# Optimization experiments

Hardware: AMD Instinct MI355X
Metric: run time of the kernel (lower is better)

## Reference

```python
import math
import jax, jax.numpy as jnp
import numpy as np

B, T, D, K, R, KC = 4, 2048, 1024, 8, 16, 4
H = 4 * D  # mlp hidden


def setup_inputs() -> dict:
    key = jax.random.key(0)
    ks = jax.random.split(key, 12)
    s = lambda i, shape: jax.random.normal(ks[i], shape, jnp.float32) * 0.02
    # state_decay_logit init: geometric decays in [dmin, dmax], logit = log(p) - log1p(-p)
    dmin, dmax = 0.9, 0.999
    dec = np.exp(np.linspace(math.log(dmin), math.log(dmax), K))
    decay_logit = jnp.asarray(np.log(dec) - np.log1p(-dec), jnp.float32)
    return dict(
        x=jax.random.normal(ks[0], (B, T, D), jnp.float32),
        conv_w=s(1, (D, 1, KC)),            # depthwise conv kernel (torch Conv1d weight)
        gp_w=s(2, (D, D)), gp_b=jnp.zeros((D,), jnp.float32),
        up_w=s(3, (D, H)), up_b=jnp.zeros((H,), jnp.float32),
        dn_w=s(4, (H, D)), dn_b=jnp.zeros((D,), jnp.float32),
        si_w=s(5, (D, K * D)),              # state_in (no bias)
        so_w=s(6, (K * D, D)),              # state_out (no bias)
        decay_logit=decay_logit,
        rs_w=s(7, (D, R)), rs_b=jnp.zeros((R,), jnp.float32),
        rwg_w=s(8, (D, 1)), rwg_b=jnp.zeros((1,), jnp.float32),
        rv_w=s(9, (D, D)), rv_b=jnp.zeros((D,), jnp.float32),
        gr_w=s(10, (D, 1)), gr_b=jnp.zeros((1,), jnp.float32),
        gl_w=s(11, (D, 1)), gl_b=jnp.zeros((1,), jnp.float32),
    )


def _rms_norm(x, eps=1e-6):
    return x * jax.lax.rsqrt(jnp.mean(x * x, axis=-1, keepdims=True) + eps)


def _forward(x, conv_w, gp_w, gp_b, up_w, up_b, dn_w, dn_b, si_w, so_w,
             decay_logit, rs_w, rs_b, rwg_w, rwg_b, rv_w, rv_b, gr_w, gr_b, gl_w, gl_b):
    Bx, Tx, Dx = x.shape
    u = _rms_norm(x)
    # --- local mixer: causal depthwise conv + sigmoid gate + SiLU MLP ---
    xc = jax.lax.conv_general_dilated(
        jnp.swapaxes(u, 1, 2), conv_w, window_strides=(1,),
        padding=[(KC - 1, 0)], feature_group_count=Dx,
        dimension_numbers=('NCH', 'OIH', 'NCH'))
    xc = jnp.swapaxes(xc, 1, 2)                       # (B,T,D) causal conv output
    xg = xc * jax.nn.sigmoid(xc @ gp_w + gp_b)
    local = jax.nn.silu(xg @ up_w + up_b) @ dn_w + dn_b
    # --- per-channel exponential-decay state + register read/write scan ---
    dec = jax.nn.sigmoid(decay_logit)                 # (K,)
    z = (u @ si_w).reshape(Bx, Tx, K, Dx)             # state_in, (B,T,K,D)
    sel = jax.nn.softmax(u @ rs_w + rs_b, axis=-1)    # soft register address (B,T,R)
    wg = jax.nn.sigmoid(u @ rwg_w + rwg_b)            # write gate (B,T,1)
    v = u @ rv_w + rv_b                                # register value (B,T,D)

    def step(carry, inp):
        s, regs = carry
        z_t, sel_t, w_t, v_t = inp
        read = jnp.einsum('br,brd->bd', sel_t, regs)  # soft read before write
        ws = (w_t * sel_t)[:, :, None]                # (B,R,1)
        regs = regs * (1.0 - ws) + ws * v_t[:, None, :]
        s = dec[None, :, None] * s + z_t
        return (s, regs), (s, read)

    init = (jnp.zeros((Bx, K, Dx), x.dtype), jnp.zeros((Bx, R, Dx), x.dtype))
    tm = lambda a: jnp.swapaxes(a, 0, 1)              # time-major for scan
    _, (s_all, reads) = jax.lax.scan(step, init, (tm(z), tm(sel), tm(wg), tm(v)))
    s_all = tm(s_all)                                 # (B,T,K,D)
    reads = tm(reads)                                 # (B,T,D)
    long_out = jnp.einsum('btkd,kde->bte', s_all, so_w.reshape(K, Dx, Dx))
    g_long = jax.nn.sigmoid(u @ gl_w + gl_b)
    g_reg = jax.nn.sigmoid(u @ gr_w + gr_b)
    return x + local + g_long * long_out + g_reg * reads


def reference(x, conv_w, gp_w, gp_b, up_w, up_b, dn_w, dn_b, si_w, so_w,
              decay_logit, rs_w, rs_b, rwg_w, rwg_b, rv_w, rv_b, gr_w, gr_b, gl_w, gl_b):
    return _forward(x, conv_w, gp_w, gp_b, up_w, up_b, dn_w, dn_b, si_w, so_w,
                    decay_logit, rs_w, rs_b, rwg_w, rwg_b, rv_w, rv_b, gr_w, gr_b, gl_w, gl_b)
```

## Files before the change

### kernel.cpp

```cpp
#include <hip/hip_runtime.h>

typedef unsigned short u16;
typedef __bf16 bf16x8 __attribute__((ext_vector_type(8)));
typedef float f32x4 __attribute__((ext_vector_type(4)));
typedef u16 u16x4 __attribute__((ext_vector_type(4)));

#define D_ 1024
#define T_ 2048
#define B_ 4
#define K_ 8
#define R_ 16
#define H_ 4096
#define NROW (B_*T_)
#define CH 32
#define CL (T_/CH)
#define CHS 64
#define CLS (T_/CHS)

__device__ __forceinline__ u16 f2bf(float f){
  union{float f;unsigned u;} v; v.f=f;
  unsigned r = v.u + 0x7FFFu + ((v.u>>16)&1u);
  return (u16)(r>>16);
}
__device__ __forceinline__ float bf2f(u16 b){
  union{unsigned u;float f;} v; v.u = ((unsigned)b)<<16; return v.f;
}
__device__ __forceinline__ float sigm(float x){ return 1.f/(1.f+__expf(-x)); }

__device__ __forceinline__ void gload_lds16(const void* g, void* l){
  __builtin_amdgcn_global_load_lds((const __attribute__((address_space(1))) void*)g,
                                   (__attribute__((address_space(3))) void*)l, 16, 0, 0);
}

__global__ __launch_bounds__(256) void fill_k(float* __restrict__ out, long n, float v){
  long i = (long)blockIdx.x*256 + threadIdx.x;
  if (i < n) out[i] = v;
}

__global__ __launch_bounds__(256) void transpose_cast(const float* __restrict__ in, u16* __restrict__ out,
                                                      int R, int C){
  __shared__ float tile[32][33];
  int bx = blockIdx.x*32;
  int by = blockIdx.y*32;
  int tx = threadIdx.x & 31, ty = threadIdx.x >> 5;
  #pragma unroll
  for (int i=0;i<32;i+=8) tile[ty+i][tx] = in[(size_t)(by+ty+i)*C + bx+tx];
  __syncthreads();
  #pragma unroll
  for (int i=0;i<32;i+=8) out[(size_t)(bx+ty+i)*R + by+tx] = f2bf(tile[tx][ty+i]);
}

__global__ __launch_bounds__(256) void castbf(const float* __restrict__ in, u16* __restrict__ out, long n){
  long i = (long)blockIdx.x*256 + threadIdx.x;
  if (i < n) out[i] = f2bf(in[i]);
}

__global__ __launch_bounds__(256) void initout_k(const float* __restrict__ x, const float* __restrict__ b,
                                                 float* __restrict__ out){
  size_t i = ((size_t)blockIdx.x*256 + threadIdx.x)*4;
  f32x4 xv = *(const f32x4*)(x + i);
  f32x4 bv = *(const f32x4*)(b + (i & (D_-1)));
  xv += bv;
  *(f32x4*)(out + i) = xv;
}

__global__ __launch_bounds__(256) void rmsnorm_k(const float* __restrict__ x, u16* __restrict__ u){
  int row = blockIdx.x;
  const float* xr = x + (size_t)row*D_;
  float xv[4]; float ss = 0.f;
  #pragma unroll
  for (int i=0;i<4;i++){ xv[i] = xr[threadIdx.x + 256*i]; ss += xv[i]*xv[i]; }
  #pragma unroll
  for (int o=32;o>0;o>>=1) ss += __shfl_down(ss, o);
  __shared__ float red[4];
  if ((threadIdx.x&63)==0) red[threadIdx.x>>6] = ss;
  __syncthreads();
  float tot = red[0]+red[1]+red[2]+red[3];
  float r = rsqrtf(tot*(1.f/D_) + 1e-6f);
  #pragma unroll
  for (int i=0;i<4;i++) u[(size_t)row*D_ + threadIdx.x + 256*i] = f2bf(xv[i]*r);
}

__global__ __launch_bounds__(256) void conv_k(const u16* __restrict__ u, const float* __restrict__ w,
                                              u16* __restrict__ xc){
  size_t base = ((size_t)blockIdx.x*256 + threadIdx.x)*4;
  int t  = (int)((base >> 10) & (T_-1));
  int d0 = (int)(base & (D_-1));
  f32x4 wv[4];
  #pragma unroll
  for (int jj=0;jj<4;jj++) wv[jj] = *(const f32x4*)&w[(d0+jj)*4];
  float acc[4] = {0.f,0.f,0.f,0.f};
  #pragma unroll
  for (int j=0;j<4;j++){
    if (t-3+j >= 0){
      u16x4 uv = *(const u16x4*)(u + base + (long)(j-3)*D_);
      #pragma unroll
      for (int jj=0;jj<4;jj++) acc[jj] += bf2f(uv[jj]) * wv[jj][j];
    }
  }
  u16x4 o;
  #pragma unroll
  for (int jj=0;jj<4;jj++) o[jj] = f2bf(acc[jj]);
  *(u16x4*)(xc + base) = o;
}

__global__ __launch_bounds__(256) void smalln_k(const u16* __restrict__ u,
    const float* __restrict__ rs_w, const float* __restrict__ rs_b,
    const float* __restrict__ rwg_w, const float* __restrict__ rwg_b,
    const float* __restrict__ gl_w, const float* __restrict__ gl_b,
    const float* __restrict__ gr_w, const float* __restrict__ gr_b,
    float* __restrict__ sel, float* __restrict__ wg, float* __restrict__ gl, float* __restrict__ gr){
  int row = blockIdx.x, tid = threadIdx.x;
  float p[19];
  #pragma unroll
  for (int c=0;c<19;c++) p[c] = 0.f;
  for (int i=0;i<4;i++){
    int e = tid + i*256;
    float ue = bf2f(u[(size_t)row*D_ + e]);
    const float* rw = rs_w + (size_t)e*16;
    #pragma unroll
    for (int r=0;r<16;r++) p[r] += ue*rw[r];
    p[16] += ue*rwg_w[e];
    p[17] += ue*gl_w[e];
    p[18] += ue*gr_w[e];
  }
  __shared__ float red[19*4];
  #pragma unroll
  for (int c=0;c<19;c++){
    float v = p[c];
    #pragma unroll
    for (int o=32;o>0;o>>=1) v += __shfl_down(v, o);
    if ((tid&63)==0) red[c*4 + (tid>>6)] = v;
  }
  __syncthreads();
  if (tid==0){
    float s[19];
    #pragma unroll
    for (int c=0;c<19;c++) s[c] = red[c*4]+red[c*4+1]+red[c*4+2]+red[c*4+3];
    float mx = -1e30f;
    #pragma unroll
    for (int r=0;r<16;r++){ s[r] += rs_b[r]; mx = fmaxf(mx, s[r]); }
    float ssum = 0.f;
    #pragma unroll
    for (int r=0;r<16;r++){ s[r] = __expf(s[r]-mx); ssum += s[r]; }
    float inv = 1.f/ssum;
    #pragma unroll
    for (int r=0;r<16;r++) sel[(size_t)row*16+r] = s[r]*inv;
    wg[row] = sigm(s[16] + rwg_b[0]);
    gl[row] = sigm(s[17] + gl_b[0]);
    gr[row] = sigm(s[18] + gr_b[0]);
  }
}

#define BM 128
#define BN 128
#define BK 32

template<int EPI>
__global__ __launch_bounds__(256)
void gemm_bt(const u16* __restrict__ A, const u16* __restrict__ BT,
             void* __restrict__ outp, const float* __restrict__ bias,
             const void* __restrict__ aux,
             int K, int lda, int ldb, int ldc,
             long zA, long zB, long zC)
{
  __shared__ __attribute__((aligned(16))) u16 As[BM*BK];
  __shared__ __attribute__((aligned(16))) u16 Bs[BN*BK];
  int nwg = gridDim.x*gridDim.y;
  int bx = blockIdx.x, by = blockIdx.y;
  if ((nwg & 7) == 0){
    int bid = blockIdx.y*gridDim.x + blockIdx.x;
    int cpx = nwg >> 3;
    int s = (bid & 7)*cpx + (bid >> 3);
    bx = s % gridDim.x; by = s / gridDim.x;
  }
  const u16* Ab = A + (size_t)blockIdx.z*zA + (size_t)bx*BM*lda;
  const u16* Bb = BT + (size_t)blockIdx.z*zB + (size_t)by*BN*ldb;
  int tid = threadIdx.x, lane = tid&63, wid = tid>>6;
  int wr = wid>>1, wc = wid&1;
  f32x4 acc[4][4];
  #pragma unroll
  for (int m=0;m<4;m++)
    #pragma unroll
    for (int n=0;n<4;n++) acc[m][n] = (f32x4){0.f,0.f,0.f,0.f};

  int srow = lane>>2;
  int scol = (lane&3)*8;
  int klo  = (lane>>4)*8;
  for (int k0=0; k0<K; k0+=BK){
    #pragma unroll
    for (int i=0;i<2;i++){
      int r0 = wid*32 + i*16;
      gload_lds16(Ab + (size_t)(r0+srow)*lda + k0 + scol, &As[r0*BK]);
      gload_lds16(Bb + (size_t)(r0+srow)*ldb + k0 + scol, &Bs[r0*BK]);
    }
    __syncthreads();
    bf16x8 af[4], bfr[4];
    #pragma unroll
    for (int m=0;m<4;m++) af[m] = *(const bf16x8*)&As[(wr*64+m*16+(lane&15))*BK + klo];
    #pragma unroll
    for (int n=0;n<4;n++) bfr[n] = *(const bf16x8*)&Bs[(wc*64+n*16+(lane&15))*BK + klo];
    #pragma unroll
    for (int m=0;m<4;m++)
      #pragma unroll
      for (int n=0;n<4;n++)
        acc[m][n] = __builtin_amdgcn_mfma_f32_16x16x32_bf16(af[m], bfr[n], acc[m][n], 0, 0, 0);
    __syncthreads();
  }

  size_t obase = (size_t)blockIdx.z*zC;
  int row0 = bx*BM + wr*64;
  int col0 = by*BN + wc*64;
  #pragma unroll
  for (int m=0;m<4;m++){
    #pragma unroll
    for (int n=0;n<4;n++){
      int col = col0 + n*16 + (lane&15);
      #pragma unroll
      for (int r=0;r<4;r++){
        int row = row0 + m*16 + (lane>>4)*4 + r;
        float c = acc[m][n][r];
        size_t idx = obase + (size_t)row*ldc + col;
        if (EPI==0){ ((u16*)outp)[idx] = f2bf(c); }
        else if (EPI==1){ ((u16*)outp)[idx] = f2bf(c + bias[col]); }
        else if (EPI==2){ float t=c+bias[col]; ((u16*)outp)[idx] = f2bf(bf2f(((const u16*)aux)[idx]) * sigm(t)); }
        else if (EPI==3){ float t=c+bias[col]; ((u16*)outp)[idx] = f2bf(t*sigm(t)); }
        else if (EPI==4){ ((float*)outp)[idx] = ((const float*)aux)[idx] + c + bias[col]; }
        else            { ((float*)outp)[idx] += c; }
      }
    }
  }
}

template<int NT, int EPI>
__global__ __launch_bounds__(512, 2)
void gemm8p(const u16* __restrict__ A, const u16* __restrict__ BT,
            void* __restrict__ outp, const float* __restrict__ bias,
            const void* __restrict__ aux,
            int lda, int ldb, int ldc, long zA, long zB, long zC,
            int rx, int ry, int nry)
{
  __shared__ __attribute__((aligned(16))) u16 lds8[65536];
  int bid = blockIdx.y*gridDim.x + blockIdx.x;
  int xcd = bid & 7;
  int s   = bid >> 3;
  int rgx = xcd / nry, rgy = xcd - rgx*nry;
  int bx = rgx*rx + (s % rx);
  int by = rgy*ry + (s / rx);

  const u16* Ab = A + (size_t)blockIdx.z*zA + (size_t)bx*256*lda;
  const u16* Bb = BT + (size_t)blockIdx.z*zB + (size_t)by*256*ldb;

  int tid = threadIdx.x, l = tid&63, w = tid>>6;
  int wr = w>>2, wc = w&3;
  int rS0 = (w*2+0)*8 + (l>>3);
  int rS1 = (w*2+1)*8 + (l>>3);
  int cg  = (((l&7) ^ (l>>3)) << 3);
  int seg0 = (w*2+0)*512;
  int seg1 = (w*2+1)*512;

  auto STAGE = [&](int h){
    int kt = h>>2, idx = h&3, par = kt&1;
    int koff = kt*64;
    if (idx < 2){
      const u16* s0 = Bb + (size_t)(idx*128 + rS0)*ldb + koff + cg;
      const u16* s1 = Bb + (size_t)(idx*128 + rS1)*ldb + koff + cg;
      u16* d = &lds8[par*32768 + 16384 + idx*8192];
      gload_lds16(s0, d + seg0);
      gload_lds16(s1, d + seg1);
    } else {
      int a = idx-2;
      const u16* s0 = Ab + (size_t)(a*128 + rS0)*lda + koff + cg;
      const u16* s1 = Ab + (size_t)(a*128 + rS1)*lda + koff + cg;
      u16* d = &lds8[par*32768 + a*8192];
      gload_lds16(s0, d + seg0);
      gload_lds16(s1, d + seg1);
    }
  };

  f32x4 acc[8][4];
  #pragma unroll
  for (int m=0;m<8;m++)
    #pragma unroll
    for (int n=0;n<4;n++) acc[m][n] = (f32x4){0.f,0.f,0.f,0.f};

  for (int h=0; h<7; ++h) STAGE(h);
  asm volatile("s_waitcnt vmcnt(6)" ::: "memory");
  __builtin_amdgcn_s_barrier();

  for (int it=0; it<NT/2; ++it){
    #pragma unroll
    for (int sub=0; sub<2; ++sub){
      int kt = it*2+sub;
      const int par = sub;
      u16* Abase = &lds8[par*32768 + wr*8192];
      u16* Bbase = &lds8[par*32768 + 16384 + (wc>>1)*8192];
      bf16x8 bf[4][2];
      #pragma unroll
      for (int q=0; q<4; ++q){
        bf16x8 af[2][2];
        if (q==0){
          #pragma unroll
          for (int n=0;n<4;n++)
            #pragma unroll
            for (int ss=0;ss<2;ss++){
              int rr = (wc&1)*64 + n*16 + (l&15);
              int c16 = (l>>4) + ss*4;
              bf[n][ss] = *(const bf16x8*)&Bbase[rr*64 + ((c16 ^ (rr&7))<<3)];
            }
        }
        #pragma unroll
        for (int i=0;i<2;i++)
          #pragma unroll
          for (int ss=0;ss<2;ss++){
            int rr = q*32 + i*16 + (l&15);
            int c16 = (l>>4) + ss*4;
            af[i][ss] = *(const bf16x8*)&Abase[rr*64 + ((c16 ^ (rr&7))<<3)];
          }
        __builtin_amdgcn_sched_barrier(0);
        int h = kt*4 + q + 7;
        if (h < 4*NT) STAGE(h);
        __builtin_amdgcn_s_barrier();
        asm volatile("s_waitcnt lgkmcnt(0)" ::: "memory");
        __builtin_amdgcn_sched_barrier(0);
        __builtin_amdgcn_s_setprio(1);
        #pragma unroll
        for (int i=0;i<2;i++)
          #pragma unroll
          for (int n=0;n<4;n++)
            #pragma unroll
            for (int ss=0;ss<2;ss++)
              acc[q*2+i][n] = __builtin_amdgcn_mfma_f32_16x16x32_bf16(af[i][ss], bf[n][ss], acc[q*2+i][n], 0, 0, 0);
        __builtin_amdgcn_s_setprio(0);
        if (q==3){
          if (kt == NT-2)      asm volatile("s_waitcnt vmcnt(0)" ::: "memory");
          else if (kt < NT-2)  asm volatile("s_waitcnt vmcnt(6)" ::: "memory");
        }
        __builtin_amdgcn_s_barrier();
      }
    }
  }

  size_t obase = (size_t)blockIdx.z*zC;
  int row0 = bx*256 + wr*128;
  int col0 = by*256 + wc*64;
  #pragma unroll
  for (int m=0;m<8;m++){
    #pragma unroll
    for (int n=0;n<4;n++){
      int col = col0 + n*16 + (l&15);
      #pragma unroll
      for (int r=0;r<4;r++){
        int row = row0 + m*16 + (l>>4)*4 + r;
        float c = acc[m][n][r];
        size_t idx = obase + (size_t)row*ldc + col;
        if (EPI==0){ ((u16*)outp)[idx] = f2bf(c); }
        else if (EPI==1){ ((u16*)outp)[idx] = f2bf(c + bias[col]); }
        else if (EPI==2){ float t=c+bias[col]; ((u16*)outp)[idx] = f2bf(bf2f(((const u16*)aux)[idx]) * sigm(t)); }
        else if (EPI==3){ float t=c+bias[col]; ((u16*)outp)[idx] = f2bf(t*sigm(t)); }
        else            { unsafeAtomicAdd(&((float*)outp)[idx], c); }
      }
    }
  }
}

template<int NT>
__global__ __launch_bounds__(512, 2)
void gemm8z(const u16* __restrict__ A, const u16* __restrict__ BT,
            void* __restrict__ outp, const float* __restrict__ bias,
            const float* __restrict__ bias2, const void* __restrict__ aux,
            int lda, int ldb, int ldc, long zA, long zB, long zC,
            int rx, int ry, int nry)
{
  __shared__ __attribute__((aligned(16))) u16 lds8[65536];
  int bid = blockIdx.y*gridDim.x + blockIdx.x;
  int xcd = bid & 7;
  int s   = bid >> 3;
  int rgx = xcd / nry, rgy = xcd - rgx*nry;
  int bx = rgx*rx + (s % rx);
  int by = rgy*ry + (s / rx);

  const u16* Ab = A + (size_t)blockIdx.z*zA + (size_t)bx*256*lda;
  const u16* Bb = BT + (size_t)blockIdx.z*zB + (size_t)by*256*ldb;

  int tid = threadIdx.x, l = tid&63, w = tid>>6;
  int wr = w>>2, wc = w&3;
  int rS0 = (w*2+0)*8 + (l>>3);
  int rS1 = (w*2+1)*8 + (l>>3);
  int cg  = (((l&7) ^ (l>>3)) << 3);
  int seg0 = (w*2+0)*512;
  int seg1 = (w*2+1)*512;

  auto STAGE = [&](int h){
    int kt = h>>2, idx = h&3, par = kt&1;
    int koff = kt*64;
    if (idx < 2){
      const u16* s0 = Bb + (size_t)(idx*128 + rS0)*ldb + koff + cg;
      const u16* s1 = Bb + (size_t)(idx*128 + rS1)*ldb + koff + cg;
      u16* d = &lds8[par*32768 + 16384 + idx*8192];
      gload_lds16(s0, d + seg0);
      gload_lds16(s1, d + seg1);
    } else {
      int a = idx-2;
      const u16* s0 = Ab + (size_t)(a*128 + rS0)*lda + koff + cg;
      const u16* s1 = Ab + (size_t)(a*128 + rS1)*lda + koff + cg;
      u16* d = &lds8[par*32768 + a*8192];
      gload_lds16(s0, d + seg0);
      gload_lds16(s1, d + seg1);
    }
  };

  f32x4 acc[8][4];
  #pragma unroll
  for (int m=0;m<8;m++)
    #pragma unroll
    for (int n=0;n<4;n++) acc[m][n] = (f32x4){0.f,0.f,0.f,0.f};

  for (int h=0; h<7; ++h) STAGE(h);
  asm volatile("s_waitcnt vmcnt(6)" ::: "memory");
  __builtin_amdgcn_s_barrier();

  for (int it=0; it<NT/2; ++it){
    #pragma unroll
    for (int sub=0; sub<2; ++sub){
      int kt = it*2+sub;
      const int par = sub;
      u16* Abase = &lds8[par*32768 + wr*8192];
      u16* Bbase = &lds8[par*32768 + 16384 + (wc>>1)*8192];
      bf16x8 bf[4][2];
      #pragma unroll
      for (int q=0; q<4; ++q){
        bf16x8 af[2][2];
        if (q==0){
          #pragma unroll
          for (int n=0;n<4;n++)
            #pragma unroll
            for (int ss=0;ss<2;ss++){
              int rr = (wc&1)*64 + n*16 + (l&15);
              int c16 = (l>>4) + ss*4;
              bf[n][ss] = *(const bf16x8*)&Bbase[rr*64 + ((c16 ^ (rr&7))<<3)];
            }
        }
        #pragma unroll
        for (int i=0;i<2;i++)
          #pragma unroll
          for (int ss=0;ss<2;ss++){
            int rr = q*32 + i*16 + (l&15);
            int c16 = (l>>4) + ss*4;
            af[i][ss] = *(const bf16x8*)&Abase[rr*64 + ((c16 ^ (rr&7))<<3)];
          }
        __builtin_amdgcn_sched_barrier(0);
        int h = kt*4 + q + 7;
        if (h < 4*NT) STAGE(h);
        __builtin_amdgcn_s_barrier();
        asm volatile("s_waitcnt lgkmcnt(0)" ::: "memory");
        __builtin_amdgcn_sched_barrier(0);
        __builtin_amdgcn_s_setprio(1);
        #pragma unroll
        for (int i=0;i<2;i++)
          #pragma unroll
          for (int n=0;n<4;n++)
            #pragma unroll
            for (int ss=0;ss<2;ss++)
              acc[q*2+i][n] = __builtin_amdgcn_mfma_f32_16x16x32_bf16(af[i][ss], bf[n][ss], acc[q*2+i][n], 0, 0, 0);
        __builtin_amdgcn_s_setprio(0);
        if (q==3){
          if (kt == NT-2)      asm volatile("s_waitcnt vmcnt(0)" ::: "memory");
          else if (kt < NT-2)  asm volatile("s_waitcnt vmcnt(6)" ::: "memory");
        }
        __builtin_amdgcn_s_barrier();
      }
    }
  }

  size_t obase = (size_t)blockIdx.z*zC;
  int row0 = bx*256 + wr*128;
  int col0 = by*256 + wc*64;
  bool z0 = (blockIdx.z == 0);
  #pragma unroll
  for (int m=0;m<8;m++){
    #pragma unroll
    for (int n=0;n<4;n++){
      int col = col0 + n*16 + (l&15);
      #pragma unroll
      for (int r=0;r<4;r++){
        int row = row0 + m*16 + (l>>4)*4 + r;
        float c = acc[m][n][r];
        size_t idx = obase + (size_t)row*ldc + col;
        if (z0){ float t=c+bias[col]; ((u16*)outp)[idx] = f2bf(bf2f(((const u16*)aux)[idx]) * sigm(t)); }
        else   { ((u16*)outp)[idx] = f2bf(c + bias2[col]); }
      }
    }
  }
}

template<int NT, int EPI>
__global__ __launch_bounds__(512, 2)
void gemm4p(const u16* __restrict__ A, const u16* __restrict__ BT,
            void* __restrict__ outp, const float* __restrict__ bias,
            const void* __restrict__ aux,
            int lda, int ldb, int ldc, long zA, long zB, long zC,
            int rx, int ry, int nry)
{
  __shared__ __attribute__((aligned(16))) u16 lds8[65536];
  int bid = blockIdx.y*gridDim.x + blockIdx.x;
  int xcd = bid & 7;
  int s   = bid >> 3;
  int rgx = xcd / nry, rgy = xcd - rgx*nry;
  int bx = rgx*rx + (s % rx);
  int by = rgy*ry + (s / rx);

  const u16* Ab = A + (size_t)blockIdx.z*zA + (size_t)bx*256*lda;
  const u16* Bb = BT + (size_t)blockIdx.z*zB + (size_t)by*256*ldb;

  int tid = threadIdx.x, l = tid&63, w = tid>>6;
  int wr = w>>2, wc = w&3;
  int rS0 = (w*2+0)*8 + (l>>3);
  int rS1 = (w*2+1)*8 + (l>>3);
  int cg  = (((l&7) ^ (l>>3)) << 3);
  int seg0 = (w*2+0)*512;
  int seg1 = (w*2+1)*512;

  auto STAGE = [&](int h){
    if (h >= 4*NT) return;
    int kt = h>>2, idx = h&3, par = kt&1;
    int koff = kt*64;
    if (idx < 2){
      const u16* s0 = Bb + (size_t)(idx*128 + rS0)*ldb + koff + cg;
      const u16* s1 = Bb + (size_t)(idx*128 + rS1)*ldb + koff + cg;
      u16* d = &lds8[par*32768 + 16384 + idx*8192];
      gload_lds16(s0, d + seg0);
      gload_lds16(s1, d + seg1);
    } else {
      int a = idx-2;
      const u16* s0 = Ab + (size_t)(a*128 + rS0)*lda + koff + cg;
      const u16* s1 = Ab + (size_t)(a*128 + rS1)*lda + koff + cg;
      u16* d = &lds8[par*32768 + a*8192];
      gload_lds16(s0, d + seg0);
      gload_lds16(s1, d + seg1);
    }
  };

  f32x4 acc[8][4];
  #pragma unroll
  for (int m=0;m<8;m++)
    #pragma unroll
    for (int n=0;n<4;n++) acc[m][n] = (f32x4){0.f,0.f,0.f,0.f};

  for (int h=0; h<7; ++h) STAGE(h);
  asm volatile("s_waitcnt vmcnt(6)" ::: "memory");
  __builtin_amdgcn_s_barrier();

  for (int kt=0; kt<NT; ++kt){
    const int par = kt&1;
    u16* Abase = &lds8[par*32768 + wr*8192];
    u16* Bbase = &lds8[par*32768 + 16384 + (wc>>1)*8192];
    bf16x8 bf[4][2];
    #pragma unroll
    for (int n=0;n<4;n++)
      #pragma unroll
      for (int ss=0;ss<2;ss++){
        int rr = (wc&1)*64 + n*16 + (l&15);
        int c16 = (l>>4) + ss*4;
        bf[n][ss] = *(const bf16x8*)&Bbase[rr*64 + ((c16 ^ (rr&7))<<3)];
      }
    bf16x8 afA[2][2][2];
    #pragma unroll
    for (int qq=0;qq<2;qq++)
      #pragma unroll
      for (int i=0;i<2;i++)
        #pragma unroll
        for (int ss=0;ss<2;ss++){
          int rr = qq*32 + i*16 + (l&15);
          int c16 = (l>>4) + ss*4;
          afA[qq][i][ss] = *(const bf16x8*)&Abase[rr*64 + ((c16 ^ (rr&7))<<3)];
        }
    STAGE(kt*4 + 7);
    STAGE(kt*4 + 8);
    __builtin_amdgcn_s_barrier();
    asm volatile("s_waitcnt lgkmcnt(0)" ::: "memory");
    __builtin_amdgcn_sched_barrier(0);
    __builtin_amdgcn_s_setprio(1);
    #pragma unroll
    for (int qq=0;qq<2;qq++)
      #pragma unroll
      for (int i=0;i<2;i++)
        #pragma unroll
        for (int n=0;n<4;n++)
          #pragma unroll
          for (int ss=0;ss<2;ss++)
            acc[qq*2+i][n] = __builtin_amdgcn_mfma_f32_16x16x32_bf16(afA[qq][i][ss], bf[n][ss], acc[qq*2+i][n], 0, 0, 0);
    __builtin_amdgcn_s_setprio(0);
    __builtin_amdgcn_s_barrier();
    bf16x8 afB[2][2][2];
    #pragma unroll
    for (int qq=0;qq<2;qq++)
      #pragma unroll
      for (int i=0;i<2;i++)
        #pragma unroll
        for (int ss=0;ss<2;ss++){
          int rr = (qq+2)*32 + i*16 + (l&15);
          int c16 = (l>>4) + ss*4;
          afB[qq][i][ss] = *(const bf16x8*)&Abase[rr*64 + ((c16 ^ (rr&7))<<3)];
        }
    STAGE(kt*4 + 9);
    STAGE(kt*4 + 10);
    __builtin_amdgcn_s_barrier();
    asm volatile("s_waitcnt lgkmcnt(0)" ::: "memory");
    __builtin_amdgcn_sched_barrier(0);
    __builtin_amdgcn_s_setprio(1);
    #pragma unroll
    for (int qq=0;qq<2;qq++)
      #pragma unroll
      for (int i=0;i<2;i++)
        #pragma unroll
        for (int n=0;n<4;n++)
          #pragma unroll
          for (int ss=0;ss<2;ss++)
            acc[(qq+2)*2+i][n] = __builtin_amdgcn_mfma_f32_16x16x32_bf16(afB[qq][i][ss], bf[n][ss], acc[(qq+2)*2+i][n], 0, 0, 0);
    __builtin_amdgcn_s_setprio(0);
    if (kt == NT-2)      asm volatile("s_waitcnt vmcnt(0)" ::: "memory");
    else if (kt < NT-2)  asm volatile("s_waitcnt vmcnt(6)" ::: "memory");
    __builtin_amdgcn_s_barrier();
  }

  size_t obase = (size_t)blockIdx.z*zC;
  int row0 = bx*256 + wr*128;
  int col0 = by*256 + wc*64;
  #pragma unroll
  for (int m=0;m<8;m++){
    #pragma unroll
    for (int n=0;n<4;n++){
      int col = col0 + n*16 + (l&15);
      #pragma unroll
      for (int r=0;r<4;r++){
        int row = row0 + m*16 + (l>>4)*4 + r;
        float c = acc[m][n][r];
        size_t idx = obase + (size_t)row*ldc + col;
        if (EPI==0){ ((u16*)outp)[idx] = f2bf(c); }
        else if (EPI==1){ ((u16*)outp)[idx] = f2bf(c + bias[col]); }
        else if (EPI==3){ float t=c+bias[col]; ((u16*)outp)[idx] = f2bf(t*sigm(t)); }
        else            { unsafeAtomicAdd(&((float*)outp)[idx], c); }
      }
    }
  }
}

template<int KH>
__global__ __launch_bounds__(256) void scan_s1k(const u16* __restrict__ y, const float* __restrict__ logit,
                                                int p, float* __restrict__ Hend){
  int k = blockIdx.x;
  int e0 = threadIdx.x*4;
  int c = blockIdx.y, b = blockIdx.z;
  float dec = sigm(logit[KH*p+k]);
  f32x4 h = (f32x4){0.f,0.f,0.f,0.f};
  size_t row0 = (size_t)b*T_ + (size_t)c*CLS;
  for (int t=0;t<CLS;t++){
    u16x4 w = *(const u16x4*)(y + (row0+t)*(size_t)(KH*D_) + (size_t)k*D_ + e0);
    #pragma unroll
    for (int j=0;j<4;j++) h[j] = dec*h[j] + bf2f(w[j]);
  }
  *(f32x4*)&Hend[(((size_t)b*CHS+c)*KH+k)*D_ + e0] = h;
}

template<int KH>
__global__ __launch_bounds__(256) void scan_s2v(const float* __restrict__ Hend, const float* __restrict__ logit,
                                                int p, float* __restrict__ Sinit){
  int idx = blockIdx.x*256 + threadIdx.x;
  if (idx >= B_*KH*D_) return;
  int e = idx % D_; int kh = (idx/D_) % KH; int b = idx/(D_*KH);
  float dec = sigm(logit[KH*p+kh]);
  float dL = powf(dec, (float)CLS);
  float carry = 0.f;
  for (int c=0;c<CHS;c++){
    size_t i3 = (((size_t)b*CHS+c)*KH+kh)*D_ + e;
    Sinit[i3] = carry;
    carry = dL*carry + Hend[i3];
  }
}

template<int KH>
__global__ __launch_bounds__(128) void scan_s3v(const u16* __restrict__ y, const float* __restrict__ logit,
                                                int p, const float* __restrict__ Sinit,
                                                const float* __restrict__ glb, float* __restrict__ out){
  int e0 = (blockIdx.x*128 + threadIdx.x)*4;
  int c = blockIdx.y, b = blockIdx.z;
  float dec[KH]; f32x4 h[KH];
  #pragma unroll
  for (int k=0;k<KH;k++){
    dec[k] = sigm(logit[KH*p+k]);
    h[k] = *(const f32x4*)&Sinit[(((size_t)b*CHS+c)*KH+k)*D_ + e0];
  }
  size_t row0 = (size_t)b*T_ + (size_t)c*CLS;
  for (int t=0;t<CLS;t++){
    const u16* yp = y + (row0+t)*(size_t)(KH*D_) + e0;
    f32x4 sum = (f32x4){0.f,0.f,0.f,0.f};
    #pragma unroll
    for (int k=0;k<KH;k++){
      u16x4 w = *(const u16x4*)(yp + (size_t)k*D_);
      #pragma unroll
      for (int j=0;j<4;j++){ h[k][j] = dec[k]*h[k][j] + bf2f(w[j]); sum[j] += h[k][j]; }
    }
    float g = glb[row0+t];
    f32x4* op = (f32x4*)&out[(row0+t)*D_ + e0];
    f32x4 ov = *op;
    #pragma unroll
    for (int j=0;j<4;j++) ov[j] += g*sum[j];
    *op = ov;
  }
}

__global__ __launch_bounds__(256) void scan_r1(const u16* __restrict__ v, const float* __restrict__ sel,
                                               const float* __restrict__ wg,
                                               float* __restrict__ Rend, float* __restrict__ Pout){
  int d = blockIdx.x*256 + threadIdx.x;
  int c = blockIdx.y, b = blockIdx.z;
  __shared__ float sel_s[CL*R_];
  __shared__ float wg_s[CL];
  size_t row0 = (size_t)b*T_ + (size_t)c*CL;
  for (int i=threadIdx.x; i<CL*R_; i+=256) sel_s[i] = sel[row0*R_ + i];
  for (int i=threadIdx.x; i<CL;    i+=256) wg_s[i]  = wg[row0 + i];
  __syncthreads();
  float regs[R_], P[R_];
  #pragma unroll
  for (int r=0;r<R_;r++){ regs[r]=0.f; P[r]=1.f; }
  for (int t=0;t<CL;t++){
    float vv = bf2f(v[(row0+t)*D_ + d]);
    float w = wg_s[t];
    #pragma unroll
    for (int r=0;r<R_;r++){
      float ws = w*sel_s[t*R_+r];
      regs[r] += ws*(vv - regs[r]);
      P[r] *= (1.f - ws);
    }
  }
  #pragma unroll
  for (int r=0;r<R_;r++) Rend[(((size_t)b*CH+c)*R_+r)*D_ + d] = regs[r];
  if (blockIdx.x==0 && threadIdx.x==0){
    #pragma unroll
    for (int r=0;r<R_;r++) Pout[((size_t)b*CH+c)*R_ + r] = P[r];
  }
}

__global__ __launch_bounds__(256) void scan_r2(const float* __restrict__ Rend, const float* __restrict__ Pbuf,
                                               float* __restrict__ Rinit){
  int idx = blockIdx.x*256 + threadIdx.x;
  if (idx >= B_*D_) return;
  int d = idx % D_; int b = idx / D_;
  float regs[R_];
  #pragma unroll
  for (int r=0;r<R_;r++) regs[r] = 0.f;
  for (int c=0;c<CH;c++){
    #pragma unroll
    for (int r=0;r<R_;r++){
      size_t i3 = (((size_t)b*CH+c)*R_+r)*D_ + d;
      Rinit[i3] = regs[r];
      regs[r] = Pbuf[((size_t)b*CH+c)*R_+r]*regs[r] + Rend[i3];
    }
  }
}

__global__ __launch_bounds__(256) void scan_r3(const u16* __restrict__ v, const float* __restrict__ sel,
                                               const float* __restrict__ wg, const float* __restrict__ Rinit,
                                               const float* __restrict__ grb, float* __restrict__ out){
  int d = blockIdx.x*256 + threadIdx.x;
  int c = blockIdx.y, b = blockIdx.z;
  __shared__ float sel_s[CL*R_];
  __shared__ float wg_s[CL];
  size_t row0 = (size_t)b*T_ + (size_t)c*CL;
  for (int i=threadIdx.x; i<CL*R_; i+=256) sel_s[i] = sel[row0*R_ + i];
  for (int i=threadIdx.x; i<CL;    i+=256) wg_s[i]  = wg[row0 + i];
  __syncthreads();
  float regs[R_];
  #pragma unroll
  for (int r=0;r<R_;r++) regs[r] = Rinit[(((size_t)b*CH+c)*R_+r)*D_ + d];
  for (int t=0;t<CL;t++){
    float vv = bf2f(v[(row0+t)*D_ + d]);
    float w = wg_s[t];
    float read = 0.f;
    #pragma unroll
    for (int r=0;r<R_;r++){
      float sr = sel_s[t*R_+r];
      read += sr*regs[r];
      float ws = w*sr;
      regs[r] += ws*(vv - regs[r]);
    }
    out[(row0+t)*D_ + d] += grb[row0+t]*read;
  }
}

static void launch_gemm(int epi, dim3 g, const u16* A, const u16* BT, void* out,
                        const float* bias, const void* aux, int K, int lda, int ldb, int ldc,
                        long zA, long zB, long zC, hipStream_t s){
  switch(epi){
    case 0: gemm_bt<0><<<g,256,0,s>>>(A,BT,out,bias,aux,K,lda,ldb,ldc,zA,zB,zC); break;
    case 1: gemm_bt<1><<<g,256,0,s>>>(A,BT,out,bias,aux,K,lda,ldb,ldc,zA,zB,zC); break;
    case 2: gemm_bt<2><<<g,256,0,s>>>(A,BT,out,bias,aux,K,lda,ldb,ldc,zA,zB,zC); break;
    case 3: gemm_bt<3><<<g,256,0,s>>>(A,BT,out,bias,aux,K,lda,ldb,ldc,zA,zB,zC); break;
    case 4: gemm_bt<4><<<g,256,0,s>>>(A,BT,out,bias,aux,K,lda,ldb,ldc,zA,zB,zC); break;
    default: gemm_bt<5><<<g,256,0,s>>>(A,BT,out,bias,aux,K,lda,ldb,ldc,zA,zB,zC); break;
  }
}

extern "C" void kernel_launch(void* const* d_in, const int* in_sizes, int n_in,
                              void* d_out, int out_size, void* d_ws, size_t ws_size,
                              hipStream_t stream){
  const float* x      = (const float*)d_in[0];
  const float* conv_w = (const float*)d_in[1];
  const float* gp_w   = (const float*)d_in[2];
  const float* gp_b   = (const float*)d_in[3];
  const float* up_w   = (const float*)d_in[4];
  const float* up_b   = (const float*)d_in[5];
  const float* dn_w   = (const float*)d_in[6];
  const float* dn_b   = (const float*)d_in[7];
  const float* si_w   = (const float*)d_in[8];
  const float* so_w   = (const float*)d_in[9];
  const float* logit  = (const float*)d_in[10];
  const float* rs_w   = (const float*)d_in[11];
  const float* rs_b   = (const float*)d_in[12];
  const float* rwg_w  = (const float*)d_in[13];
  const float* rwg_b  = (const float*)d_in[14];
  const float* rv_w   = (const float*)d_in[15];
  const float* rv_b   = (const float*)d_in[16];
  const float* gr_w   = (const float*)d_in[17];
  const float* gr_b   = (const float*)d_in[18];
  const float* gl_w   = (const float*)d_in[19];
  const float* gl_b   = (const float*)d_in[20];
  float* out = (float*)d_out;
  char* base = (char*)d_ws;

  {
    size_t off = 0;
    auto al = [&](size_t b)->char*{ char* r = base+off; off += (b+255)&~(size_t)255; return r; };
    char* u_r    = al((size_t)NROW*D_*2);
    char* v_r    = al((size_t)NROW*D_*2);
    char* big    = al((size_t)121634816);
    float* sel   = (float*)al((size_t)NROW*R_*4);
    float* wgb   = (float*)al((size_t)NROW*4);
    float* glb   = (float*)al((size_t)NROW*4);
    float* grb   = (float*)al((size_t)NROW*4);
    float* Pbuf  = (float*)al((size_t)B_*CH*R_*4);
    float* Rend  = (float*)al((size_t)B_*CH*R_*D_*4);
    float* Rinit = (float*)al((size_t)B_*CH*R_*D_*4);
    if (off <= ws_size){
      u16* u_bf  = (u16*)u_r;
      u16* v_bf  = (u16*)v_r;
      u16* hid   = (u16*)big;
      u16* xc_bf = (u16*)(big + (size_t)67108864);
      u16* xg_bf = (u16*)(big + (size_t)83886080);
      u16* gpT   = (u16*)(big + (size_t)100663296);
      u16* upT   = (u16*)(big + (size_t)102760448);
      u16* dnT   = (u16*)(big + (size_t)111149056);
      u16* rvT   = (u16*)(big + (size_t)119537664);
      u16* WT    = (u16*)big;
      u16* si_bf = (u16*)(big + (size_t)16777216);
      u16* soT   = (u16*)(big + (size_t)33554432);
      u16* y_bf  = (u16*)(big + (size_t)16777216);
      float* Hend  = (float*)(big + (size_t)83886080);
      float* Sinit = (float*)(big + (size_t)88080384);

      transpose_cast<<<dim3(D_/32, D_/32),256,0,stream>>>(gp_w, gpT, D_, D_);
      transpose_cast<<<dim3(H_/32, D_/32),256,0,stream>>>(up_w, upT, D_, H_);
      transpose_cast<<<dim3(D_/32, H_/32),256,0,stream>>>(dn_w, dnT, H_, D_);
      transpose_cast<<<dim3(D_/32, D_/32),256,0,stream>>>(rv_w, rvT, D_, D_);

      rmsnorm_k<<<NROW,256,0,stream>>>(x, u_bf);
      conv_k<<<(NROW*D_)/1024,256,0,stream>>>(u_bf, conv_w, xc_bf);
      smalln_k<<<NROW,256,0,stream>>>(u_bf, rs_w, rs_b, rwg_w, rwg_b, gl_w, gl_b, gr_w, gr_b,
                                      sel, wgb, glb, grb);

      gemm8z<16><<<dim3(NROW/256, D_/256, 2), 512, 0, stream>>>(
          xc_bf, gpT, xg_bf, gp_b, rv_b, xc_bf, D_, D_, D_,
          (long)(u_bf - xc_bf), (long)(rvT - gpT), (long)(v_bf - xg_bf), 4, 4, 1);

      gemm8p<16,3><<<dim3(NROW/256, H_/256), 512, 0, stream>>>(
          xg_bf, upT, hid, up_b, nullptr, D_, D_, H_, 0, 0, 0, 8, 8, 2);

      initout_k<<<(NROW*D_)/1024,256,0,stream>>>(x, dn_b, out);
      gemm8p<32,5><<<dim3(NROW/256, D_/256, 2), 512, 0, stream>>>(
          hid, dnT, out, nullptr, nullptr, H_, H_, D_, 2048, 2048, 0, 4, 4, 1);

      transpose_cast<<<dim3(D_/32, (K_*D_)/32),256,0,stream>>>(so_w, soT, K_*D_, D_);
      castbf<<<((long)D_*K_*D_+255)/256,256,0,stream>>>(si_w, si_bf, (long)D_*K_*D_);
      gemm8p<16,0><<<dim3(D_/256, D_/256, K_), 512, 0, stream>>>(
          soT, si_bf, WT, nullptr, nullptr, K_*D_, K_*D_, D_, (long)D_, (long)D_, (long)D_*D_, 2, 1, 4);

      {
        int h = 0;
        gemm4p<16,0><<<dim3(NROW/256, (4*D_)/256), 512, 0, stream>>>(
            u_bf, WT + (size_t)h*4*D_*D_, y_bf, nullptr, nullptr, D_, D_, 4*D_, 0, 0, 0, 8, 8, 2);
        scan_s1k<4><<<dim3(4, CHS, B_),256,0,stream>>>(y_bf, logit, h, Hend);
        scan_s2v<4><<<(B_*4*D_+255)/256,256,0,stream>>>(Hend, logit, h, Sinit);
        scan_s3v<4><<<dim3(2, CHS, B_),128,0,stream>>>(y_bf, logit, h, Sinit, glb, out);
      }
      {
        int h = 1;
        gemm8p<16,0><<<dim3(NROW/256, (4*D_)/256), 512, 0, stream>>>(
            u_bf, WT + (size_t)h*4*D_*D_, y_bf, nullptr, nullptr, D_, D_, 4*D_, 0, 0, 0, 8, 8, 2);
        scan_s1k<4><<<dim3(4, CHS, B_),256,0,stream>>>(y_bf, logit, h, Hend);
        scan_s2v<4><<<(B_*4*D_+255)/256,256,0,stream>>>(Hend, logit, h, Sinit);
        scan_s3v<4><<<dim3(2, CHS, B_),128,0,stream>>>(y_bf, logit, h, Sinit, glb, out);
      }

      scan_r1<<<dim3(D_/256, CH, B_),256,0,stream>>>(v_bf, sel, wgb, Rend, Pbuf);
      scan_r2<<<(B_*D_+255)/256,256,0,stream>>>(Rend, Pbuf, Rinit);
      scan_r3<<<dim3(D_/256, CH, B_),256,0,stream>>>(v_bf, sel, wgb, Rinit, grb, out);
      return;
    }
  }

  const size_t MB16_8 = (size_t)NROW*D_*2;
  size_t off = 0;
  auto alloc = [&](size_t bytes)->char*{
    char* r = base + off; off += (bytes + 255) & ~(size_t)255; return r;
  };
  char* R0 = alloc(MB16_8);
  char* R1 = alloc(MB16_8);
  char* R2 = alloc(2*MB16_8);
  char* R3 = alloc((size_t)21*1024*1024);
  float* sel  = (float*)alloc((size_t)NROW*R_*4);
  float* wgb  = (float*)alloc((size_t)NROW*4);
  float* glb  = (float*)alloc((size_t)NROW*4);
  float* grb  = (float*)alloc((size_t)NROW*4);
  float* Pbuf = (float*)alloc((size_t)B_*CH*R_*4);
  float* Hend = (float*)alloc((size_t)B_*CHS*2*D_*4);
  float* Sinit= (float*)alloc((size_t)B_*CHS*2*D_*4);
  if (off > ws_size){
    fill_k<<<((long)out_size+255)/256,256,0,stream>>>(out, out_size, 12345.0f);
    return;
  }

  u16* u_bf  = (u16*)R0;
  u16* v_bf  = (u16*)R1;
  u16* xc_bf = (u16*)R2;
  u16* xg_bf = (u16*)(R2 + MB16_8);
  u16* hid_bf= (u16*)R2;
  u16* soT   = (u16*)R2;
  u16* si_bf = (u16*)(R2 + MB16_8);
  u16* y_bf  = (u16*)R2;
  u16* gpT   = (u16*)R3;
  u16* upT   = (u16*)(R3 + (size_t)2*1024*1024 + 131072);
  u16* dnT   = (u16*)(R3 + (size_t)10*1024*1024 + 655360);
  u16* rvT   = (u16*)(R3 + (size_t)19*1024*1024);
  u16* WT    = (u16*)R3;
  float* Rend = (float*)R3;
  float* Rinit= (float*)(R3 + (size_t)NROW*D_);

  transpose_cast<<<dim3(D_/32, D_/32),256,0,stream>>>(gp_w, gpT, D_, D_);
  transpose_cast<<<dim3(H_/32, D_/32),256,0,stream>>>(up_w, upT, D_, H_);
  transpose_cast<<<dim3(D_/32, H_/32),256,0,stream>>>(dn_w, dnT, H_, D_);
  transpose_cast<<<dim3(D_/32, D_/32),256,0,stream>>>(rv_w, rvT, D_, D_);

  rmsnorm_k<<<NROW,256,0,stream>>>(x, u_bf);
  conv_k<<<(NROW*D_)/1024,256,0,stream>>>(u_bf, conv_w, xc_bf);
  smalln_k<<<NROW,256,0,stream>>>(u_bf, rs_w, rs_b, rwg_w, rwg_b, gl_w, gl_b, gr_w, gr_b,
                                  sel, wgb, glb, grb);

  launch_gemm(2, dim3(NROW/BM, D_/BN, 1), xc_bf, gpT, xg_bf, gp_b, xc_bf,
              D_, D_, D_, D_, 0, 0, 0, stream);
  launch_gemm(1, dim3(NROW/BM, D_/BN, 1), u_bf, rvT, v_bf, rv_b, nullptr,
              D_, D_, D_, D_, 0, 0, 0, stream);
  for (int q=0; q<4; q++){
    launch_gemm(3, dim3(NROW/BM, 1024/BN, 1), xg_bf, upT + (size_t)q*1024*D_, hid_bf,
                up_b + q*1024, nullptr, D_, D_, D_, 1024, 0, 0, 0, stream);
    launch_gemm(q==0?4:5, dim3(NROW/BM, D_/BN, 1), hid_bf, dnT + (size_t)q*1024, out,
                dn_b, x, 1024, 1024, H_, D_, 0, 0, 0, stream);
  }

  transpose_cast<<<dim3(D_/32, (K_*D_)/32),256,0,stream>>>(so_w, soT, K_*D_, D_);
  castbf<<<((long)D_*K_*D_+255)/256,256,0,stream>>>(si_w, si_bf, (long)D_*K_*D_);
  launch_gemm(0, dim3(D_/BM, D_/BN, K_), soT, si_bf, WT, nullptr, nullptr,
              D_, K_*D_, K_*D_, D_, (long)D_, (long)D_, (long)D_*D_, stream);

  for (int p=0; p<4; p++){
    launch_gemm(0, dim3(NROW/BM, (2*D_)/BN, 1), u_bf, WT + (size_t)(2*p)*D_*D_, y_bf,
                nullptr, nullptr, D_, D_, D_, 2*D_, 0, 0, 0, stream);
    scan_s1k<2><<<dim3(2, CHS, B_),256,0,stream>>>(y_bf, logit, p, Hend);
    scan_s2v<2><<<(B_*2*D_+255)/256,256,0,stream>>>(Hend, logit, p, Sinit);
    scan_s3v<2><<<dim3(2, CHS, B_),128,0,stream>>>(y_bf, logit, p, Sinit, glb, out);
  }

  scan_r1<<<dim3(D_/256, CH, B_),256,0,stream>>>(v_bf, sel, wgb, Rend, Pbuf);
  scan_r2<<<(B_*D_+255)/256,256,0,stream>>>(Rend, Pbuf, Rinit);
  scan_r3<<<dim3(D_/256, CH, B_),256,0,stream>>>(v_bf, sel, wgb, Rinit, grb, out);
}
```

Baseline: 712.9 us.

## Replace gemm4p with 256x128-tile triple-buffered GEMM for up-proj and state-in

```diff
diff --git a/kernel.cpp b/kernel.cpp
--- a/kernel.cpp
+++ b/kernel.cpp
@@ -495,14 +495,14 @@
 }
 
 template<int NT, int EPI>
-__global__ __launch_bounds__(512, 2)
-void gemm4p(const u16* __restrict__ A, const u16* __restrict__ BT,
+__global__ __launch_bounds__(256, 2)
+void gemm3b(const u16* __restrict__ A, const u16* __restrict__ BT,
             void* __restrict__ outp, const float* __restrict__ bias,
             const void* __restrict__ aux,
             int lda, int ldb, int ldc, long zA, long zB, long zC,
             int rx, int ry, int nry)
 {
-  __shared__ __attribute__((aligned(16))) u16 lds8[65536];
+  __shared__ __attribute__((aligned(16))) u16 lds3[3*12288];
   int bid = blockIdx.y*gridDim.x + blockIdx.x;
   int xcd = bid & 7;
   int s   = bid >> 3;
@@ -511,33 +511,26 @@
   int by = rgy*ry + (s / rx);
 
   const u16* Ab = A + (size_t)blockIdx.z*zA + (size_t)bx*256*lda;
-  const u16* Bb = BT + (size_t)blockIdx.z*zB + (size_t)by*256*ldb;
+  const u16* Bb = BT + (size_t)blockIdx.z*zB + (size_t)by*128*ldb;
 
   int tid = threadIdx.x, l = tid&63, w = tid>>6;
-  int wr = w>>2, wc = w&3;
-  int rS0 = (w*2+0)*8 + (l>>3);
-  int rS1 = (w*2+1)*8 + (l>>3);
-  int cg  = (((l&7) ^ (l>>3)) << 3);
-  int seg0 = (w*2+0)*512;
-  int seg1 = (w*2+1)*512;
-
-  auto STAGE = [&](int h){
-    if (h >= 4*NT) return;
-    int kt = h>>2, idx = h&3, par = kt&1;
-    int koff = kt*64;
-    if (idx < 2){
-      const u16* s0 = Bb + (size_t)(idx*128 + rS0)*ldb + koff + cg;
-      const u16* s1 = Bb + (size_t)(idx*128 + rS1)*ldb + koff + cg;
-      u16* d = &lds8[par*32768 + 16384 + idx*8192];
-      gload_lds16(s0, d + seg0);
-      gload_lds16(s1, d + seg1);
-    } else {
-      int a = idx-2;
-      const u16* s0 = Ab + (size_t)(a*128 + rS0)*lda + koff + cg;
-      const u16* s1 = Ab + (size_t)(a*128 + rS1)*lda + koff + cg;
-      u16* d = &lds8[par*32768 + a*8192];
-      gload_lds16(s0, d + seg0);
-      gload_lds16(s1, d + seg1);
+  int wr = w>>1, wc = w&1;
+  int lq = l>>2, lc8 = (l&3)*8;
+
+  auto STAGE = [&](int kt){
+    int buf = kt%3;
+    int koff = kt*32;
+    u16* Adst = &lds3[buf*12288];
+    u16* Bdst = &lds3[buf*12288 + 8192];
+    #pragma unroll
+    for (int c=0;c<4;c++){
+      int row = (w*4+c)*16 + lq;
+      gload_lds16(Ab + (size_t)row*lda + koff + lc8, Adst + (w*4+c)*512);
+    }
+    #pragma unroll
+    for (int c=0;c<2;c++){
+      int row = (w*2+c)*16 + lq;
+      gload_lds16(Bb + (size_t)row*ldb + koff + lc8, Bdst + (w*2+c)*512);
     }
   };
 
@@ -547,86 +540,42 @@
     #pragma unroll
     for (int n=0;n<4;n++) acc[m][n] = (f32x4){0.f,0.f,0.f,0.f};
 
-  for (int h=0; h<7; ++h) STAGE(h);
-  asm volatile("s_waitcnt vmcnt(6)" ::: "memory");
-  __builtin_amdgcn_s_barrier();
+  STAGE(0);
+  STAGE(1);
 
   for (int kt=0; kt<NT; ++kt){
-    const int par = kt&1;
-    u16* Abase = &lds8[par*32768 + wr*8192];
-    u16* Bbase = &lds8[par*32768 + 16384 + (wc>>1)*8192];
-    bf16x8 bf[4][2];
-    #pragma unroll
-    for (int n=0;n<4;n++)
+    if (kt+2 < NT) STAGE(kt+2);
+    if (kt < NT-2)      asm volatile("s_waitcnt vmcnt(12)" ::: "memory");
+    else if (kt == NT-2) asm volatile("s_waitcnt vmcnt(6)" ::: "memory");
+    else                 asm volatile("s_waitcnt vmcnt(0)" ::: "memory");
+    __builtin_amdgcn_s_barrier();
+    int buf = kt%3;
+    const u16* Asrc = &lds3[buf*12288];
+    const u16* Bsrc = &lds3[buf*12288 + 8192];
+    bf16x8 bf[4], af[8];
+    #pragma unroll
+    for (int n=0;n<4;n++){
+      int rr = wc*64 + n*16 + (l&15);
+      bf[n] = *(const bf16x8*)&Bsrc[rr*32 + (l>>4)*8];
+    }
+    #pragma unroll
+    for (int m=0;m<8;m++){
+      int rr = wr*128 + m*16 + (l&15);
+      af[m] = *(const bf16x8*)&Asrc[rr*32 + (l>>4)*8];
+    }
+    __builtin_amdgcn_s_setprio(1);
+    #pragma unroll
+    for (int m=0;m<8;m++)
       #pragma unroll
-      for (int ss=0;ss<2;ss++){
-        int rr = (wc&1)*64 + n*16 + (l&15);
-        int c16 = (l>>4) + ss*4;
-        bf[n][ss] = *(const bf16x8*)&Bbase[rr*64 + ((c16 ^ (rr&7))<<3)];
-      }
-    bf16x8 afA[2][2][2];
-    #pragma unroll
-    for (int qq=0;qq<2;qq++)
-      #pragma unroll
-      for (int i=0;i<2;i++)
-        #pragma unroll
-        for (int ss=0;ss<2;ss++){
-          int rr = qq*32 + i*16 + (l&15);
-          int c16 = (l>>4) + ss*4;
-          afA[qq][i][ss] = *(const bf16x8*)&Abase[rr*64 + ((c16 ^ (rr&7))<<3)];
-        }
-    STAGE(kt*4 + 7);
-    STAGE(kt*4 + 8);
-    __builtin_amdgcn_s_barrier();
-    asm volatile("s_waitcnt lgkmcnt(0)" ::: "memory");
-    __builtin_amdgcn_sched_barrier(0);
-    __builtin_amdgcn_s_setprio(1);
-    #pragma unroll
-    for (int qq=0;qq<2;qq++)
-      #pragma unroll
-      for (int i=0;i<2;i++)
-        #pragma unroll
-        for (int n=0;n<4;n++)
-          #pragma unroll
-          for (int ss=0;ss<2;ss++)
-            acc[qq*2+i][n] = __builtin_amdgcn_mfma_f32_16x16x32_bf16(afA[qq][i][ss], bf[n][ss], acc[qq*2+i][n], 0, 0, 0);
+      for (int n=0;n<4;n++)
+        acc[m][n] = __builtin_amdgcn_mfma_f32_16x16x32_bf16(af[m], bf[n], acc[m][n], 0, 0, 0);
     __builtin_amdgcn_s_setprio(0);
     __builtin_amdgcn_s_barrier();
-    bf16x8 afB[2][2][2];
-    #pragma unroll
-    for (int qq=0;qq<2;qq++)
-      #pragma unroll
-      for (int i=0;i<2;i++)
-        #pragma unroll
-        for (int ss=0;ss<2;ss++){
-          int rr = (qq+2)*32 + i*16 + (l&15);
-          int c16 = (l>>4) + ss*4;
-          afB[qq][i][ss] = *(const bf16x8*)&Abase[rr*64 + ((c16 ^ (rr&7))<<3)];
-        }
-    STAGE(kt*4 + 9);
-    STAGE(kt*4 + 10);
-    __builtin_amdgcn_s_barrier();
-    asm volatile("s_waitcnt lgkmcnt(0)" ::: "memory");
-    __builtin_amdgcn_sched_barrier(0);
-    __builtin_amdgcn_s_setprio(1);
-    #pragma unroll
-    for (int qq=0;qq<2;qq++)
-      #pragma unroll
-      for (int i=0;i<2;i++)
-        #pragma unroll
-        for (int n=0;n<4;n++)
-          #pragma unroll
-          for (int ss=0;ss<2;ss++)
-            acc[(qq+2)*2+i][n] = __builtin_amdgcn_mfma_f32_16x16x32_bf16(afB[qq][i][ss], bf[n][ss], acc[(qq+2)*2+i][n], 0, 0, 0);
-    __builtin_amdgcn_s_setprio(0);
-    if (kt == NT-2)      asm volatile("s_waitcnt vmcnt(0)" ::: "memory");
-    else if (kt < NT-2)  asm volatile("s_waitcnt vmcnt(6)" ::: "memory");
-    __builtin_amdgcn_s_barrier();
   }
 
   size_t obase = (size_t)blockIdx.z*zC;
   int row0 = bx*256 + wr*128;
-  int col0 = by*256 + wc*64;
+  int col0 = by*128 + wc*64;
   #pragma unroll
   for (int m=0;m<8;m++){
     #pragma unroll
@@ -873,8 +822,8 @@
           xc_bf, gpT, xg_bf, gp_b, rv_b, xc_bf, D_, D_, D_,
           (long)(u_bf - xc_bf), (long)(rvT - gpT), (long)(v_bf - xg_bf), 4, 4, 1);
 
-      gemm8p<16,3><<<dim3(NROW/256, H_/256), 512, 0, stream>>>(
-          xg_bf, upT, hid, up_b, nullptr, D_, D_, H_, 0, 0, 0, 8, 8, 2);
+      gemm3b<32,3><<<dim3(NROW/256, H_/128), 256, 0, stream>>>(
+          xg_bf, upT, hid, up_b, nullptr, D_, D_, H_, 0, 0, 0, 8, 16, 2);
 
       initout_k<<<(NROW*D_)/1024,256,0,stream>>>(x, dn_b, out);
       gemm8p<32,5><<<dim3(NROW/256, D_/256, 2), 512, 0, stream>>>(
@@ -887,8 +836,8 @@
 
       {
         int h = 0;
-        gemm4p<16,0><<<dim3(NROW/256, (4*D_)/256), 512, 0, stream>>>(
-            u_bf, WT + (size_t)h*4*D_*D_, y_bf, nullptr, nullptr, D_, D_, 4*D_, 0, 0, 0, 8, 8, 2);
+        gemm3b<32,0><<<dim3(NROW/256, (4*D_)/128), 256, 0, stream>>>(
+            u_bf, WT + (size_t)h*4*D_*D_, y_bf, nullptr, nullptr, D_, D_, 4*D_, 0, 0, 0, 8, 16, 2);
         scan_s1k<4><<<dim3(4, CHS, B_),256,0,stream>>>(y_bf, logit, h, Hend);
         scan_s2v<4><<<(B_*4*D_+255)/256,256,0,stream>>>(Hend, logit, h, Sinit);
         scan_s3v<4><<<dim3(2, CHS, B_),128,0,stream>>>(y_bf, logit, h, Sinit, glb, out);
```

Measured after the change: 726.3 us. No clear change (+1.9%).
